# Kernel optimization log

Hardware: AMD Instinct MI355X
Metric: run time of the kernel (lower is better)

## Reference

```python
import jax, jax.numpy as jnp
import numpy as np

N_NODES = 50000
N_EDGES = 800000
IN_CH = 128
HID = 128
LAT = 64


def setup_inputs() -> dict:
    key = jax.random.key(0)
    ks = jax.random.split(key, 8)
    s = 1.0 / np.sqrt(IN_CH)
    sh = 1.0 / np.sqrt(HID)
    x = jax.random.normal(ks[0], (N_NODES, IN_CH), dtype=jnp.float32)
    edge_index = jax.random.randint(ks[1], (2, N_EDGES), 0, N_NODES, dtype=jnp.int64)
    return {
        "x": x,
        "edge_index": edge_index,
        "W1": jax.random.normal(ks[2], (IN_CH, HID), dtype=jnp.float32) * s,
        "b1": jnp.zeros((HID,), dtype=jnp.float32),
        "W2": jax.random.normal(ks[3], (HID, HID), dtype=jnp.float32) * sh,
        "b2": jnp.zeros((HID,), dtype=jnp.float32),
        "W_mu": jax.random.normal(ks[4], (HID, LAT), dtype=jnp.float32) * sh,
        "b_mu": jnp.zeros((LAT,), dtype=jnp.float32),
        "W_lv": jax.random.normal(ks[5], (HID, LAT), dtype=jnp.float32) * sh,
        "b_lv": jnp.zeros((LAT,), dtype=jnp.float32),
    }


def _gcn_norm(edge_index, num_nodes):
    # PyG gcn_norm with add_self_loops=True: deg[i] = in-degree(i) + 1
    src, dst = edge_index[0], edge_index[1]
    deg = jax.ops.segment_sum(jnp.ones((edge_index.shape[1],), jnp.float32), dst,
                              num_segments=num_nodes) + 1.0
    dinv = 1.0 / jnp.sqrt(deg)  # deg >= 1, never inf
    edge_norm = dinv[src] * dinv[dst]          # [E]
    self_norm = dinv * dinv                    # [N] norm for self-loop edges
    return src, dst, edge_norm, self_norm


def _gcn_conv(x, W, b, src, dst, edge_norm, self_norm, num_nodes):
    h = x @ W                                           # [N, out]
    msg = h[src] * edge_norm[:, None]                   # [E, out] gather
    agg = jax.ops.segment_sum(msg, dst, num_segments=num_nodes)  # scatter-add
    agg = agg + h * self_norm[:, None]                  # self-loop contribution
    return agg + b


def reference(x, edge_index, W1, b1, W2, b2, W_mu, b_mu, W_lv, b_lv):
    n = x.shape[0]
    src, dst, e_norm, s_norm = _gcn_norm(edge_index, n)
    h = jax.nn.relu(_gcn_conv(x, W1, b1, src, dst, e_norm, s_norm, n))
    h = jax.nn.relu(_gcn_conv(h, W2, b2, src, dst, e_norm, s_norm, n))
    mu = h @ W_mu + b_mu
    logvar = h @ W_lv + b_lv
    return mu, logvar
```

## Files before the change

kernel.cpp:

```cpp
#include <hip/hip_runtime.h>

#define NN 50000
#define NE 800000
#define NSLICE 6250
#define BKT 64

typedef short s8v  __attribute__((ext_vector_type(8)));
typedef float f4v  __attribute__((ext_vector_type(4)));

__device__ __forceinline__ unsigned f2bf(float f) {
    unsigned u = __float_as_uint(f);
    return (u + 0x7fffu + ((u >> 16) & 1u)) >> 16;
}
__device__ __forceinline__ float bf2f_lo(unsigned u) { return __uint_as_float(u << 16); }
__device__ __forceinline__ float bf2f_hi(unsigned u) { return __uint_as_float(u & 0xffff0000u); }

__device__ __forceinline__ s8v pack8(float4 p, float4 q) {
    union { unsigned u[4]; s8v v; } r;
    r.u[0] = (f2bf(p.y) << 16) | f2bf(p.x);
    r.u[1] = (f2bf(p.w) << 16) | f2bf(p.z);
    r.u[2] = (f2bf(q.y) << 16) | f2bf(q.x);
    r.u[3] = (f2bf(q.w) << 16) | f2bf(q.z);
    return r.v;
}

__global__ __launch_bounds__(256) void k_prep(const float* __restrict__ W1, const float* __restrict__ W2,
                                              const float* __restrict__ Wmu, const float* __restrict__ Wlv,
                                              unsigned short* __restrict__ Wt, int* __restrict__ cursor) {
    int b = blockIdx.x;
    if (b < 192) {
        int idx = b * 256 + threadIdx.x;
        int m = idx >> 14, i = idx & 16383;
        int n = i & 127, k = i >> 7;
        float v;
        if (m == 0)      v = W1[k * 128 + n];
        else if (m == 1) v = W2[k * 128 + n];
        else             v = (n < 64) ? Wmu[k * 64 + n] : Wlv[k * 64 + (n - 64)];
        Wt[m * 16384 + n * 128 + k] = (unsigned short)f2bf(v);
    } else {
        int i = (b - 192) * 256 + threadIdx.x;
        if (i < NN) cursor[i] = 0;
    }
}

__global__ __launch_bounds__(256) void k_fg(const float4* __restrict__ x4,
                                            const unsigned short* __restrict__ Wt,
                                            unsigned short* __restrict__ Hb,
                                            const int* __restrict__ src, const int* __restrict__ dst,
                                            int* __restrict__ cursor, int* __restrict__ esrc) {
    int b = blockIdx.x;
    if (b < 782) {
        int wave = threadIdx.x >> 6, lane = threadIdx.x & 63;
        int quad = lane >> 4, l16 = lane & 15;
        int row0 = b * 64 + wave * 16;
        int arow = row0 + l16;
        int arc  = arow < NN ? arow : NN - 1;

        const float4* xq = x4 + (size_t)arc * 32;
        s8v a0 = pack8(xq[ 0 + quad * 2], xq[ 1 + quad * 2]);
        s8v a1 = pack8(xq[ 8 + quad * 2], xq[ 9 + quad * 2]);
        s8v a2 = pack8(xq[16 + quad * 2], xq[17 + quad * 2]);
        s8v a3 = pack8(xq[24 + quad * 2], xq[25 + quad * 2]);

        f4v acc[8];
#pragma unroll
        for (int c = 0; c < 8; ++c) acc[c] = (f4v)0.f;

#pragma unroll
        for (int c = 0; c < 8; ++c) {
            const s8v* wp = (const s8v*)(Wt + (size_t)(c * 16 + l16) * 128);
            acc[c] = __builtin_amdgcn_mfma_f32_16x16x32_bf16(a0, wp[quad],      acc[c], 0, 0, 0);
            acc[c] = __builtin_amdgcn_mfma_f32_16x16x32_bf16(a1, wp[4 + quad],  acc[c], 0, 0, 0);
            acc[c] = __builtin_amdgcn_mfma_f32_16x16x32_bf16(a2, wp[8 + quad],  acc[c], 0, 0, 0);
            acc[c] = __builtin_amdgcn_mfma_f32_16x16x32_bf16(a3, wp[12 + quad], acc[c], 0, 0, 0);
        }

#pragma unroll
        for (int c = 0; c < 8; ++c) {
#pragma unroll
            for (int r = 0; r < 4; ++r) {
                int ro = row0 + quad * 4 + r;
                if (ro < NN) Hb[(size_t)ro * 128 + c * 16 + l16] = (unsigned short)f2bf(acc[c][r]);
            }
        }
    } else {
        int bb = b - 782;
        int xcd = b & 7;
        int e = (bb >> 3) * 256 + threadIdx.x;
        if (e >= NE) return;
        int d = dst[e];
        if (d / NSLICE != xcd) return;
        int s = src[e];
        int p = atomicAdd(&cursor[d], 1);
        if (p < BKT) esrc[(size_t)d * BKT + p] = s;
    }
}

__global__ __launch_bounds__(256) void k_gemm(const unsigned short* __restrict__ Xb,
                                              const unsigned short* __restrict__ Wt,
                                              unsigned short* __restrict__ Cb, int N) {
    int wave = threadIdx.x >> 6, lane = threadIdx.x & 63;
    int quad = lane >> 4, l16 = lane & 15;
    int row0 = blockIdx.x * 64 + wave * 16;
    int arow = row0 + l16;
    int arc  = arow < N ? arow : N - 1;

    const s8v* xp = (const s8v*)(Xb + (size_t)arc * 128);
    s8v a0 = xp[quad], a1 = xp[4 + quad], a2 = xp[8 + quad], a3 = xp[12 + quad];

    f4v acc[8];
#pragma unroll
    for (int c = 0; c < 8; ++c) acc[c] = (f4v)0.f;

#pragma unroll
    for (int c = 0; c < 8; ++c) {
        const s8v* wp = (const s8v*)(Wt + (size_t)(c * 16 + l16) * 128);
        acc[c] = __builtin_amdgcn_mfma_f32_16x16x32_bf16(a0, wp[quad],      acc[c], 0, 0, 0);
        acc[c] = __builtin_amdgcn_mfma_f32_16x16x32_bf16(a1, wp[4 + quad],  acc[c], 0, 0, 0);
        acc[c] = __builtin_amdgcn_mfma_f32_16x16x32_bf16(a2, wp[8 + quad],  acc[c], 0, 0, 0);
        acc[c] = __builtin_amdgcn_mfma_f32_16x16x32_bf16(a3, wp[12 + quad], acc[c], 0, 0, 0);
    }

#pragma unroll
    for (int c = 0; c < 8; ++c) {
#pragma unroll
        for (int r = 0; r < 4; ++r) {
            int ro = row0 + quad * 4 + r;
            if (ro < N) Cb[(size_t)ro * 128 + c * 16 + l16] = (unsigned short)f2bf(acc[c][r]);
        }
    }
}

__global__ __launch_bounds__(256) void k_final(const unsigned short* __restrict__ Xb,
                                               const unsigned short* __restrict__ Wt,
                                               const float* __restrict__ bmu, const float* __restrict__ blv,
                                               float* __restrict__ out, int N) {
    int wave = threadIdx.x >> 6, lane = threadIdx.x & 63;
    int quad = lane >> 4, l16 = lane & 15;
    int row0 = blockIdx.x * 64 + wave * 16;
    int arow = row0 + l16;
    int arc  = arow < N ? arow : N - 1;

    const s8v* xp = (const s8v*)(Xb + (size_t)arc * 128);
    s8v a0 = xp[quad], a1 = xp[4 + quad], a2 = xp[8 + quad], a3 = xp[12 + quad];

    f4v acc[8];
#pragma unroll
    for (int c = 0; c < 8; ++c) acc[c] = (f4v)0.f;

#pragma unroll
    for (int c = 0; c < 8; ++c) {
        const s8v* wp = (const s8v*)(Wt + (size_t)(c * 16 + l16) * 128);
        acc[c] = __builtin_amdgcn_mfma_f32_16x16x32_bf16(a0, wp[quad],      acc[c], 0, 0, 0);
        acc[c] = __builtin_amdgcn_mfma_f32_16x16x32_bf16(a1, wp[4 + quad],  acc[c], 0, 0, 0);
        acc[c] = __builtin_amdgcn_mfma_f32_16x16x32_bf16(a2, wp[8 + quad],  acc[c], 0, 0, 0);
        acc[c] = __builtin_amdgcn_mfma_f32_16x16x32_bf16(a3, wp[12 + quad], acc[c], 0, 0, 0);
    }

#pragma unroll
    for (int c = 0; c < 8; ++c) {
        int col  = c * 16 + l16;
        float bb = (col < 64) ? bmu[col] : blv[col - 64];
#pragma unroll
        for (int r = 0; r < 4; ++r) {
            int ro = row0 + quad * 4 + r;
            if (ro < N) {
                float v = acc[c][r] + bb;
                if (col < 64) out[(size_t)ro * 64 + col] = v;
                else          out[(size_t)NN * 64 + (size_t)ro * 64 + (col - 64)] = v;
            }
        }
    }
}

template<bool FIRST>
__global__ __launch_bounds__(256) void k_agg(const unsigned short* __restrict__ hb,
                                             const int* __restrict__ degc,
                                             const int* __restrict__ esrc,
                                             float* __restrict__ dinv,
                                             const float* __restrict__ b,
                                             unsigned short* __restrict__ outb) {
    int lane = threadIdx.x & 63;
    int n = blockIdx.x * 4 + (threadIdx.x >> 6);
    int d = __builtin_amdgcn_readfirstlane(degc[n]);
    float dn;
    if (FIRST) {
        dn = rsqrtf((float)(d + 1));
        if (lane == 0) dinv[n] = dn;
    } else {
        dn = __uint_as_float(__builtin_amdgcn_readfirstlane(__float_as_uint(dinv[n])));
    }
    const unsigned* h2 = (const unsigned*)hb;
    const int* bk = esrc + (size_t)n * BKT;
    int sv = bk[lane];

    float ax0 = 0.f, ay0 = 0.f, ax1 = 0.f, ay1 = 0.f;
    float ax2 = 0.f, ay2 = 0.f, ax3 = 0.f, ay3 = 0.f;

    {
        unsigned u[24];
        float    w[24];
#pragma unroll
        for (int k = 0; k < 24; ++k) {
            int sraw = __builtin_amdgcn_readlane(sv, k);
            unsigned su = ((unsigned)sraw < (unsigned)NN) ? (unsigned)sraw : 0u;
            float ws;
            if (FIRST) {
                int cs = __builtin_amdgcn_readfirstlane(degc[su]);
                ws = rsqrtf((float)(cs + 1));
            } else {
                ws = __uint_as_float(__builtin_amdgcn_readfirstlane(__float_as_uint(dinv[su])));
            }
            w[k] = (k < d) ? ws * dn : 0.f;
            u[k] = h2[(size_t)su * 64 + lane];
        }
#pragma unroll
        for (int k = 0; k < 24; ++k) {
            float lo = bf2f_lo(u[k]), hi = bf2f_hi(u[k]);
            switch (k & 3) {
                case 0: ax0 += lo * w[k]; ay0 += hi * w[k]; break;
                case 1: ax1 += lo * w[k]; ay1 += hi * w[k]; break;
                case 2: ax2 += lo * w[k]; ay2 += hi * w[k]; break;
                default: ax3 += lo * w[k]; ay3 += hi * w[k]; break;
            }
        }
    }

    for (int e0 = 24; e0 < d; e0 += 8) {
        unsigned u[8];
        float    w[8];
#pragma unroll
        for (int k = 0; k < 8; ++k) {
            int ek  = e0 + k;
            int ekc = ek < (BKT - 1) ? ek : (BKT - 1);
            int sraw = __builtin_amdgcn_readlane(sv, ekc);
            unsigned su = ((unsigned)sraw < (unsigned)NN) ? (unsigned)sraw : 0u;
            float ws;
            if (FIRST) {
                int cs = __builtin_amdgcn_readfirstlane(degc[su]);
                ws = rsqrtf((float)(cs + 1));
            } else {
                ws = __uint_as_float(__builtin_amdgcn_readfirstlane(__float_as_uint(dinv[su])));
            }
            w[k] = (ek < d) ? ws * dn : 0.f;
            u[k] = h2[(size_t)su * 64 + lane];
        }
#pragma unroll
        for (int k = 0; k < 8; ++k) {
            float lo = bf2f_lo(u[k]), hi = bf2f_hi(u[k]);
            switch (k & 3) {
                case 0: ax0 += lo * w[k]; ay0 += hi * w[k]; break;
                case 1: ax1 += lo * w[k]; ay1 += hi * w[k]; break;
                case 2: ax2 += lo * w[k]; ay2 += hi * w[k]; break;
                default: ax3 += lo * w[k]; ay3 += hi * w[k]; break;
            }
        }
    }

    float sn = dn * dn;
    unsigned uh = h2[(size_t)n * 64 + lane];
    float2 bb = ((const float2*)b)[lane];
    float rx = fmaxf((ax0 + ax1) + (ax2 + ax3) + bf2f_lo(uh) * sn + bb.x, 0.f);
    float ry = fmaxf((ay0 + ay1) + (ay2 + ay3) + bf2f_hi(uh) * sn + bb.y, 0.f);
    ((unsigned*)outb)[(size_t)n * 64 + lane] = (f2bf(ry) << 16) | f2bf(rx);
}

extern "C" void kernel_launch(void* const* d_in, const int* in_sizes, int n_in,
                              void* d_out, int out_size, void* d_ws, size_t ws_size,
                              hipStream_t stream) {
    const float* x    = (const float*)d_in[0];
    const int*   eidx = (const int*)d_in[1];
    const float* W1   = (const float*)d_in[2];
    const float* b1   = (const float*)d_in[3];
    const float* W2   = (const float*)d_in[4];
    const float* b2   = (const float*)d_in[5];
    const float* Wmu  = (const float*)d_in[6];
    const float* bmu  = (const float*)d_in[7];
    const float* Wlv  = (const float*)d_in[8];
    const float* blv  = (const float*)d_in[9];
    float* out = (float*)d_out;

    const int* src = eidx;
    const int* dst = eidx + NE;

    float*          ws     = (float*)d_ws;
    int*            cursor = (int*)ws;
    float*          dinv   = ws + 50048;
    int*            esrc   = (int*)(ws + 100096);
    unsigned short* Wt     = (unsigned short*)(ws + 3300096);
    unsigned short* Hb     = (unsigned short*)(ws + 3324672);
    unsigned short* Gb     = (unsigned short*)(ws + 6524672);

    const int gFG = 782 + ((NE + 255) / 256) * 8;
    const int gG  = (NN + 63) / 64;
    const int gA  = NN / 4;

    k_prep<<<388, 256, 0, stream>>>(W1, W2, Wmu, Wlv, Wt, cursor);

    k_fg<<<gFG, 256, 0, stream>>>((const float4*)x, Wt, Hb, src, dst, cursor, esrc);

    k_agg<true><<<gA, 256, 0, stream>>>(Hb, cursor, esrc, dinv, b1, Gb);

    k_gemm<<<gG, 256, 0, stream>>>(Gb, Wt + 16384, Hb, NN);
    k_agg<false><<<gA, 256, 0, stream>>>(Hb, cursor, esrc, dinv, b2, Gb);

    k_final<<<gG, 256, 0, stream>>>(Gb, Wt + 32768, bmu, blv, out, NN);
}
```

Before: 270.8 us.

## Aggregate before transform with channel-sliced layout and fused GEMM epilogues

Reorders each GCN layer to aggregate the bf16 features first and apply the weight matrix afterwards (A·X·W), which is valid because aggregation is linear. Features are stored in 8 channel slices of 16 bf16 values, and the aggregation kernel processes one slice per block so gathers stay within a smaller working set. Bias and ReLU move into the GEMM epilogues, and the second GEMM is fused with the mu/logvar projection through LDS. Edge bucketing now uses 16-bit source indices and vectorized int4 reads, and the XCD-sliced atomic scheme is removed. Risks include more aggregation blocks, shuffle overhead and extra rounding from aggregating before the transform.

```diff
diff --git a/kernel.cpp b/kernel.cpp
--- a/kernel.cpp
+++ b/kernel.cpp
@@ -2,7 +2,6 @@
 
 #define NN 50000
 #define NE 800000
-#define NSLICE 6250
 #define BKT 64
 
 typedef short s8v  __attribute__((ext_vector_type(8)));
@@ -14,15 +13,6 @@
 }
 __device__ __forceinline__ float bf2f_lo(unsigned u) { return __uint_as_float(u << 16); }
 __device__ __forceinline__ float bf2f_hi(unsigned u) { return __uint_as_float(u & 0xffff0000u); }
-
-__device__ __forceinline__ s8v pack8(float4 p, float4 q) {
-    union { unsigned u[4]; s8v v; } r;
-    r.u[0] = (f2bf(p.y) << 16) | f2bf(p.x);
-    r.u[1] = (f2bf(p.w) << 16) | f2bf(p.z);
-    r.u[2] = (f2bf(q.y) << 16) | f2bf(q.x);
-    r.u[3] = (f2bf(q.w) << 16) | f2bf(q.z);
-    return r.v;
-}
 
 __global__ __launch_bounds__(256) void k_prep(const float* __restrict__ W1, const float* __restrict__ W2,
                                               const float* __restrict__ Wmu, const float* __restrict__ Wlv,
@@ -43,75 +33,94 @@
     }
 }
 
-__global__ __launch_bounds__(256) void k_fg(const float4* __restrict__ x4,
-                                            const unsigned short* __restrict__ Wt,
-                                            unsigned short* __restrict__ Hb,
+__global__ __launch_bounds__(256) void k_fc(const float2* __restrict__ x2,
                                             const int* __restrict__ src, const int* __restrict__ dst,
-                                            int* __restrict__ cursor, int* __restrict__ esrc) {
+                                            int* __restrict__ cursor, unsigned short* __restrict__ esrcu,
+                                            unsigned* __restrict__ Xcs2) {
     int b = blockIdx.x;
     if (b < 782) {
-        int wave = threadIdx.x >> 6, lane = threadIdx.x & 63;
-        int quad = lane >> 4, l16 = lane & 15;
-        int row0 = b * 64 + wave * 16;
-        int arow = row0 + l16;
-        int arc  = arow < NN ? arow : NN - 1;
-
-        const float4* xq = x4 + (size_t)arc * 32;
-        s8v a0 = pack8(xq[ 0 + quad * 2], xq[ 1 + quad * 2]);
-        s8v a1 = pack8(xq[ 8 + quad * 2], xq[ 9 + quad * 2]);
-        s8v a2 = pack8(xq[16 + quad * 2], xq[17 + quad * 2]);
-        s8v a3 = pack8(xq[24 + quad * 2], xq[25 + quad * 2]);
-
-        f4v acc[8];
-#pragma unroll
-        for (int c = 0; c < 8; ++c) acc[c] = (f4v)0.f;
-
-#pragma unroll
-        for (int c = 0; c < 8; ++c) {
-            const s8v* wp = (const s8v*)(Wt + (size_t)(c * 16 + l16) * 128);
-            acc[c] = __builtin_amdgcn_mfma_f32_16x16x32_bf16(a0, wp[quad],      acc[c], 0, 0, 0);
-            acc[c] = __builtin_amdgcn_mfma_f32_16x16x32_bf16(a1, wp[4 + quad],  acc[c], 0, 0, 0);
-            acc[c] = __builtin_amdgcn_mfma_f32_16x16x32_bf16(a2, wp[8 + quad],  acc[c], 0, 0, 0);
-            acc[c] = __builtin_amdgcn_mfma_f32_16x16x32_bf16(a3, wp[12 + quad], acc[c], 0, 0, 0);
-        }
-
-#pragma unroll
-        for (int c = 0; c < 8; ++c) {
-#pragma unroll
-            for (int r = 0; r < 4; ++r) {
-                int ro = row0 + quad * 4 + r;
-                if (ro < NN) Hb[(size_t)ro * 128 + c * 16 + l16] = (unsigned short)f2bf(acc[c][r]);
-            }
+        int idx = b * 256 + (int)threadIdx.x;
+        if (idx >= NE / 4) return;
+        int4 d4 = ((const int4*)dst)[idx];
+        int4 s4 = ((const int4*)src)[idx];
+        int dv[4] = { d4.x, d4.y, d4.z, d4.w };
+        int sv[4] = { s4.x, s4.y, s4.z, s4.w };
+#pragma unroll
+        for (int k = 0; k < 4; ++k) {
+            int p = atomicAdd(&cursor[dv[k]], 1);
+            if (p < BKT) esrcu[(size_t)dv[k] * BKT + p] = (unsigned short)sv[k];
         }
     } else {
-        int bb = b - 782;
-        int xcd = b & 7;
-        int e = (bb >> 3) * 256 + threadIdx.x;
-        if (e >= NE) return;
-        int d = dst[e];
-        if (d / NSLICE != xcd) return;
-        int s = src[e];
-        int p = atomicAdd(&cursor[d], 1);
-        if (p < BKT) esrc[(size_t)d * BKT + p] = s;
-    }
-}
-
-__global__ __launch_bounds__(256) void k_gemm(const unsigned short* __restrict__ Xb,
-                                              const unsigned short* __restrict__ Wt,
-                                              unsigned short* __restrict__ Cb, int N) {
+        int t = (b - 782) * 256 + (int)threadIdx.x;
+        int n = t >> 6, dw = t & 63;
+        float2 v = x2[(size_t)n * 64 + dw];
+        Xcs2[((size_t)(dw >> 3) * NN + n) * 8 + (dw & 7)] = (f2bf(v.y) << 16) | f2bf(v.x);
+    }
+}
+
+__global__ __launch_bounds__(256) void k_agg(const unsigned* __restrict__ in2,
+                                             const int* __restrict__ degc,
+                                             const unsigned short* __restrict__ esrcu,
+                                             unsigned* __restrict__ out2) {
+    int s = blockIdx.x & 7, chunk = blockIdx.x >> 3;
+    int wv = threadIdx.x >> 6, lane = threadIdx.x & 63;
+    int g = lane >> 3, dw = lane & 7;
+    int ng = chunk * 32 + wv * 8 + g;
+    int ngc = ng < NN ? ng : NN - 1;
+
+    int dg_own = degc[ngc];
+    float dn = rsqrtf((float)(dg_own + 1));
+    int dmax = dg_own;
+    dmax = max(dmax, __shfl_xor(dmax, 8));
+    dmax = max(dmax, __shfl_xor(dmax, 16));
+    dmax = max(dmax, __shfl_xor(dmax, 32));
+    dmax = __builtin_amdgcn_readfirstlane(dmax);
+
+    const unsigned* base = in2 + (size_t)s * (NN * 8);
+    float ax = 0.f, ay = 0.f;
+
+    for (int e0 = 0; e0 < dmax; e0 += 8) {
+        int slot = e0 + dw;
+        unsigned sraw = esrcu[(size_t)ngc * BKT + slot];
+        unsigned su_l = sraw < (unsigned)NN ? sraw : 0u;
+        int dgs = degc[su_l];
+        float wl = (slot < dg_own) ? rsqrtf((float)(dgs + 1)) * dn : 0.f;
+#pragma unroll
+        for (int j = 0; j < 8; ++j) {
+            int srcLane = g * 8 + j;
+            unsigned su = (unsigned)__shfl((int)su_l, srcLane);
+            float w = __shfl(wl, srcLane);
+            unsigned u = base[(size_t)su * 8 + dw];
+            ax += bf2f_lo(u) * w; ay += bf2f_hi(u) * w;
+        }
+    }
+
+    unsigned uh = base[(size_t)ngc * 8 + dw];
+    float sn = dn * dn;
+    ax += bf2f_lo(uh) * sn; ay += bf2f_hi(uh) * sn;
+    if (ng < NN)
+        out2[(size_t)s * (NN * 8) + (size_t)ng * 8 + dw] = (f2bf(ay) << 16) | f2bf(ax);
+}
+
+__global__ __launch_bounds__(256) void k_g1(const unsigned short* __restrict__ A,
+                                            const unsigned short* __restrict__ Wt,
+                                            const float* __restrict__ b1,
+                                            unsigned short* __restrict__ C) {
     int wave = threadIdx.x >> 6, lane = threadIdx.x & 63;
     int quad = lane >> 4, l16 = lane & 15;
     int row0 = blockIdx.x * 64 + wave * 16;
     int arow = row0 + l16;
-    int arc  = arow < N ? arow : N - 1;
-
-    const s8v* xp = (const s8v*)(Xb + (size_t)arc * 128);
-    s8v a0 = xp[quad], a1 = xp[4 + quad], a2 = xp[8 + quad], a3 = xp[12 + quad];
+    int arc  = arow < NN ? arow : NN - 1;
+
+    int half = (quad & 1) * 8, sq = quad >> 1;
+    s8v a0 = *(const s8v*)(A + ((size_t)(sq    ) * NN + arc) * 16 + half);
+    s8v a1 = *(const s8v*)(A + ((size_t)(sq + 2) * NN + arc) * 16 + half);
+    s8v a2 = *(const s8v*)(A + ((size_t)(sq + 4) * NN + arc) * 16 + half);
+    s8v a3 = *(const s8v*)(A + ((size_t)(sq + 6) * NN + arc) * 16 + half);
 
     f4v acc[8];
 #pragma unroll
     for (int c = 0; c < 8; ++c) acc[c] = (f4v)0.f;
-
 #pragma unroll
     for (int c = 0; c < 8; ++c) {
         const s8v* wp = (const s8v*)(Wt + (size_t)(c * 16 + l16) * 128);
@@ -123,40 +132,81 @@
 
 #pragma unroll
     for (int c = 0; c < 8; ++c) {
+        float bb = b1[c * 16 + l16];
 #pragma unroll
         for (int r = 0; r < 4; ++r) {
             int ro = row0 + quad * 4 + r;
-            if (ro < N) Cb[(size_t)ro * 128 + c * 16 + l16] = (unsigned short)f2bf(acc[c][r]);
-        }
-    }
-}
-
-__global__ __launch_bounds__(256) void k_final(const unsigned short* __restrict__ Xb,
-                                               const unsigned short* __restrict__ Wt,
-                                               const float* __restrict__ bmu, const float* __restrict__ blv,
-                                               float* __restrict__ out, int N) {
+            if (ro < NN)
+                C[((size_t)c * NN + ro) * 16 + l16] =
+                    (unsigned short)f2bf(fmaxf(acc[c][r] + bb, 0.f));
+        }
+    }
+}
+
+__global__ __launch_bounds__(256) void k_g2p(const unsigned short* __restrict__ A,
+                                             const unsigned short* __restrict__ W2t,
+                                             const float* __restrict__ b2,
+                                             const unsigned short* __restrict__ Wpt,
+                                             const float* __restrict__ bmu, const float* __restrict__ blv,
+                                             float* __restrict__ out) {
+    __shared__ __align__(16) unsigned lds[4][16][64];
     int wave = threadIdx.x >> 6, lane = threadIdx.x & 63;
     int quad = lane >> 4, l16 = lane & 15;
     int row0 = blockIdx.x * 64 + wave * 16;
     int arow = row0 + l16;
-    int arc  = arow < N ? arow : N - 1;
-
-    const s8v* xp = (const s8v*)(Xb + (size_t)arc * 128);
-    s8v a0 = xp[quad], a1 = xp[4 + quad], a2 = xp[8 + quad], a3 = xp[12 + quad];
+    int arc  = arow < NN ? arow : NN - 1;
+
+    int half = (quad & 1) * 8, sq = quad >> 1;
+    s8v a0 = *(const s8v*)(A + ((size_t)(sq    ) * NN + arc) * 16 + half);
+    s8v a1 = *(const s8v*)(A + ((size_t)(sq + 2) * NN + arc) * 16 + half);
+    s8v a2 = *(const s8v*)(A + ((size_t)(sq + 4) * NN + arc) * 16 + half);
+    s8v a3 = *(const s8v*)(A + ((size_t)(sq + 6) * NN + arc) * 16 + half);
 
     f4v acc[8];
 #pragma unroll
     for (int c = 0; c < 8; ++c) acc[c] = (f4v)0.f;
-
-#pragma unroll
-    for (int c = 0; c < 8; ++c) {
-        const s8v* wp = (const s8v*)(Wt + (size_t)(c * 16 + l16) * 128);
+#pragma unroll
+    for (int c = 0; c < 8; ++c) {
+        const s8v* wp = (const s8v*)(W2t + (size_t)(c * 16 + l16) * 128);
         acc[c] = __builtin_amdgcn_mfma_f32_16x16x32_bf16(a0, wp[quad],      acc[c], 0, 0, 0);
         acc[c] = __builtin_amdgcn_mfma_f32_16x16x32_bf16(a1, wp[4 + quad],  acc[c], 0, 0, 0);
         acc[c] = __builtin_amdgcn_mfma_f32_16x16x32_bf16(a2, wp[8 + quad],  acc[c], 0, 0, 0);
         acc[c] = __builtin_amdgcn_mfma_f32_16x16x32_bf16(a3, wp[12 + quad], acc[c], 0, 0, 0);
     }
 
+    unsigned short* lw = (unsigned short*)&lds[wave][0][0];
+#pragma unroll
+    for (int c = 0; c < 8; ++c) {
+        float bb = b2[c * 16 + l16];
+#pragma unroll
+        for (int r = 0; r < 4; ++r) {
+            int row = quad * 4 + r;
+            int ch  = c * 16 + l16;
+            int p   = (c * 8 + (l16 >> 1)) ^ ((row & 7) << 2);
+            lw[(row * 64 + p) * 2 + (ch & 1)] =
+                (unsigned short)f2bf(fmaxf(acc[c][r] + bb, 0.f));
+        }
+    }
+
+    int kx = l16 & 7;
+    const unsigned* rowp = &lds[wave][l16][0];
+    s8v h0 = *(const s8v*)(rowp + 4 * (( 0 + quad) ^ kx));
+    s8v h1 = *(const s8v*)(rowp + 4 * (( 4 + quad) ^ kx));
+    s8v h2 = *(const s8v*)(rowp + 4 * (( 8 + quad) ^ kx));
+    s8v h3 = *(const s8v*)(rowp + 4 * ((12 + quad) ^ kx));
+
+    f4v pacc[8];
+#pragma unroll
+    for (int c = 0; c < 8; ++c) pacc[c] = (f4v)0.f;
+#pragma unroll
+    for (int c = 0; c < 8; ++c) {
+        const s8v* wp = (const s8v*)(Wpt + (size_t)(c * 16 + l16) * 128);
+        pacc[c] = __builtin_amdgcn_mfma_f32_16x16x32_bf16(h0, wp[quad],      pacc[c], 0, 0, 0);
+        pacc[c] = __builtin_amdgcn_mfma_f32_16x16x32_bf16(h1, wp[4 + quad],  pacc[c], 0, 0, 0);
+        pacc[c] = __builtin_amdgcn_mfma_f32_16x16x32_bf16(h2, wp[8 + quad],  pacc[c], 0, 0, 0);
+        pacc[c] = __builtin_amdgcn_mfma_f32_16x16x32_bf16(h3, wp[12 + quad], pacc[c], 0, 0, 0);
+    }
+
 #pragma unroll
     for (int c = 0; c < 8; ++c) {
         int col  = c * 16 + l16;
@@ -164,105 +214,13 @@
 #pragma unroll
         for (int r = 0; r < 4; ++r) {
             int ro = row0 + quad * 4 + r;
-            if (ro < N) {
-                float v = acc[c][r] + bb;
+            if (ro < NN) {
+                float v = pacc[c][r] + bb;
                 if (col < 64) out[(size_t)ro * 64 + col] = v;
                 else          out[(size_t)NN * 64 + (size_t)ro * 64 + (col - 64)] = v;
             }
         }
     }
-}
-
-template<bool FIRST>
-__global__ __launch_bounds__(256) void k_agg(const unsigned short* __restrict__ hb,
-                                             const int* __restrict__ degc,
-                                             const int* __restrict__ esrc,
-                                             float* __restrict__ dinv,
-                                             const float* __restrict__ b,
-                                             unsigned short* __restrict__ outb) {
-    int lane = threadIdx.x & 63;
-    int n = blockIdx.x * 4 + (threadIdx.x >> 6);
-    int d = __builtin_amdgcn_readfirstlane(degc[n]);
-    float dn;
-    if (FIRST) {
-        dn = rsqrtf((float)(d + 1));
-        if (lane == 0) dinv[n] = dn;
-    } else {
-        dn = __uint_as_float(__builtin_amdgcn_readfirstlane(__float_as_uint(dinv[n])));
-    }
-    const unsigned* h2 = (const unsigned*)hb;
-    const int* bk = esrc + (size_t)n * BKT;
-    int sv = bk[lane];
-
-    float ax0 = 0.f, ay0 = 0.f, ax1 = 0.f, ay1 = 0.f;
-    float ax2 = 0.f, ay2 = 0.f, ax3 = 0.f, ay3 = 0.f;
-
-    {
-        unsigned u[24];
-        float    w[24];
-#pragma unroll
-        for (int k = 0; k < 24; ++k) {
-            int sraw = __builtin_amdgcn_readlane(sv, k);
-            unsigned su = ((unsigned)sraw < (unsigned)NN) ? (unsigned)sraw : 0u;
-            float ws;
-            if (FIRST) {
-                int cs = __builtin_amdgcn_readfirstlane(degc[su]);
-                ws = rsqrtf((float)(cs + 1));
-            } else {
-                ws = __uint_as_float(__builtin_amdgcn_readfirstlane(__float_as_uint(dinv[su])));
-            }
-            w[k] = (k < d) ? ws * dn : 0.f;
-            u[k] = h2[(size_t)su * 64 + lane];
-        }
-#pragma unroll
-        for (int k = 0; k < 24; ++k) {
-            float lo = bf2f_lo(u[k]), hi = bf2f_hi(u[k]);
-            switch (k & 3) {
-                case 0: ax0 += lo * w[k]; ay0 += hi * w[k]; break;
-                case 1: ax1 += lo * w[k]; ay1 += hi * w[k]; break;
-                case 2: ax2 += lo * w[k]; ay2 += hi * w[k]; break;
-                default: ax3 += lo * w[k]; ay3 += hi * w[k]; break;
-            }
-        }
-    }
-
-    for (int e0 = 24; e0 < d; e0 += 8) {
-        unsigned u[8];
-        float    w[8];
-#pragma unroll
-        for (int k = 0; k < 8; ++k) {
-            int ek  = e0 + k;
-            int ekc = ek < (BKT - 1) ? ek : (BKT - 1);
-            int sraw = __builtin_amdgcn_readlane(sv, ekc);
-            unsigned su = ((unsigned)sraw < (unsigned)NN) ? (unsigned)sraw : 0u;
-            float ws;
-            if (FIRST) {
-                int cs = __builtin_amdgcn_readfirstlane(degc[su]);
-                ws = rsqrtf((float)(cs + 1));
-            } else {
-                ws = __uint_as_float(__builtin_amdgcn_readfirstlane(__float_as_uint(dinv[su])));
-            }
-            w[k] = (ek < d) ? ws * dn : 0.f;
-            u[k] = h2[(size_t)su * 64 + lane];
-        }
-#pragma unroll
-        for (int k = 0; k < 8; ++k) {
-            float lo = bf2f_lo(u[k]), hi = bf2f_hi(u[k]);
-            switch (k & 3) {
-                case 0: ax0 += lo * w[k]; ay0 += hi * w[k]; break;
-                case 1: ax1 += lo * w[k]; ay1 += hi * w[k]; break;
-                case 2: ax2 += lo * w[k]; ay2 += hi * w[k]; break;
-                default: ax3 += lo * w[k]; ay3 += hi * w[k]; break;
-            }
-        }
-    }
-
-    float sn = dn * dn;
-    unsigned uh = h2[(size_t)n * 64 + lane];
-    float2 bb = ((const float2*)b)[lane];
-    float rx = fmaxf((ax0 + ax1) + (ax2 + ax3) + bf2f_lo(uh) * sn + bb.x, 0.f);
-    float ry = fmaxf((ay0 + ay1) + (ay2 + ay3) + bf2f_hi(uh) * sn + bb.y, 0.f);
-    ((unsigned*)outb)[(size_t)n * 64 + lane] = (f2bf(ry) << 16) | f2bf(rx);
 }
 
 extern "C" void kernel_launch(void* const* d_in, const int* in_sizes, int n_in,
@@ -285,24 +243,24 @@
 
     float*          ws     = (float*)d_ws;
     int*            cursor = (int*)ws;
-    float*          dinv   = ws + 50048;
-    int*            esrc   = (int*)(ws + 100096);
-    unsigned short* Wt     = (unsigned short*)(ws + 3300096);
-    unsigned short* Hb     = (unsigned short*)(ws + 3324672);
-    unsigned short* Gb     = (unsigned short*)(ws + 6524672);
-
-    const int gFG = 782 + ((NE + 255) / 256) * 8;
+    unsigned short* esrcu  = (unsigned short*)(ws + 50048);
+    unsigned short* Wt     = (unsigned short*)(ws + 1650048);
+    unsigned short* bufA   = (unsigned short*)(ws + 1674624);
+    unsigned short* bufB   = (unsigned short*)(ws + 4874624);
+
+    const int gFC = 782 + 12500;
+    const int gA  = 1563 * 8;
     const int gG  = (NN + 63) / 64;
-    const int gA  = NN / 4;
 
     k_prep<<<388, 256, 0, stream>>>(W1, W2, Wmu, Wlv, Wt, cursor);
 
-    k_fg<<<gFG, 256, 0, stream>>>((const float4*)x, Wt, Hb, src, dst, cursor, esrc);
-
-    k_agg<true><<<gA, 256, 0, stream>>>(Hb, cursor, esrc, dinv, b1, Gb);
-
-    k_gemm<<<gG, 256, 0, stream>>>(Gb, Wt + 16384, Hb, NN);
-    k_agg<false><<<gA, 256, 0, stream>>>(Hb, cursor, esrc, dinv, b2, Gb);
-
-    k_final<<<gG, 256, 0, stream>>>(Gb, Wt + 32768, bmu, blv, out, NN);
-}
+    k_fc<<<gFC, 256, 0, stream>>>((const float2*)x, src, dst, cursor, esrcu, (unsigned*)bufA);
+
+    k_agg<<<gA, 256, 0, stream>>>((const unsigned*)bufA, cursor, esrcu, (unsigned*)bufB);
+
+    k_g1<<<gG, 256, 0, stream>>>(bufA == bufA ? bufB : bufB, Wt, b1, bufA);
+
+    k_agg<<<gA, 256, 0, stream>>>((const unsigned*)bufA, cursor, esrcu, (unsigned*)bufB);
+
+    k_g2p<<<gG, 256, 0, stream>>>(bufB, Wt + 16384, b2, Wt + 32768, bmu, blv, out);
+}
```

Result: slower. 333.5 us (+23.2%).
